# Performance work log

Measured on AMD Instinct MI355X. Metric: run time of the kernel, lower is better.

## Reference

```python
import jax, jax.numpy as jnp
import numpy as np

B, N, DIN, DOUT = 16, 256, 64, 64
TEMP = 2.0          # temperatures[0]
POOL_K = 0.5        # pool_ratios[0]
BN_EPS = 1e-5


def setup_inputs() -> dict:
    key = jax.random.key(0)
    ks = jax.random.split(key, 8)
    g = lambda i, shape: (jax.random.normal(ks[i], shape, jnp.float32) * 0.08)
    return {
        "x": jax.random.normal(ks[0], (B, N, DIN), jnp.float32),
        # GraphAttentionLayer params
        "W_att": g(1, (DIN, DOUT)), "b_att": jnp.zeros((DOUT,), jnp.float32),
        "att_w": g(2, (DOUT,)),                      # att_weight [DOUT,1] squeezed
        "W_pwa": g(3, (DIN, DOUT)), "b_pwa": jnp.zeros((DOUT,), jnp.float32),
        "W_pna": g(4, (DIN, DOUT)), "b_pna": jnp.zeros((DOUT,), jnp.float32),
        "bn_scale": jnp.ones((DOUT,), jnp.float32),
        "bn_bias": jnp.zeros((DOUT,), jnp.float32),
        # GraphPool params
        "pool_w": g(5, (DOUT,)), "pool_b": jnp.zeros((), jnp.float32),
    }


def reference(x, W_att, b_att, att_w, W_pwa, b_pwa, W_pna, b_pna,
              bn_scale, bn_bias, pool_w, pool_b):
    # --- GraphAttentionLayer (eval mode: dropout = identity) ---
    # pairwise node multiplication: [B, i, j, DIN]
    pm = x[:, :, None, :] * x[:, None, :, :]
    att = jnp.tanh(jnp.einsum('bijd,de->bije', pm, W_att) + b_att)   # [B,N,N,DOUT]
    logits = jnp.einsum('bije,e->bij', att, att_w) / TEMP            # [B,N,N]
    # torch softmax over dim=-2 of [B,i,j,1] == axis j (the aggregated axis)
    A = jax.nn.softmax(logits, axis=2)                               # [B,N,N]
    agg = jnp.einsum('bij,bjd->bid', A, x)                           # [B,N,DIN]
    h = (agg @ W_pwa + b_pwa) + (x @ W_pna + b_pna)                  # [B,N,DOUT]
    # BatchNorm1d eval with running_mean=0, running_var=1
    h = h * (bn_scale / jnp.sqrt(1.0 + BN_EPS)) + bn_bias
    h = jax.nn.selu(h)
    # --- GraphPool (eval mode: dropout = identity) ---
    scores = jax.nn.sigmoid(h @ pool_w + pool_b)                     # [B,N]
    k = max(int(N * POOL_K), 1)
    _, idx = jax.lax.top_k(scores, k)                                # [B,k]
    hw = h * scores[:, :, None]
    out = jnp.take_along_axis(hw, idx[:, :, None], axis=1)           # [B,k,DOUT]
    return out
```

## Files before the change

kernel.cpp:

```cpp
#include <hip/hip_runtime.h>
#include <hip/hip_bf16.h>
#include <math.h>

#define BB 16
#define NN 256
#define DD 64
#define KTOP 128

typedef short s16x8 __attribute__((ext_vector_type(8)));
typedef float f32x4 __attribute__((ext_vector_type(4)));

typedef union { s16x8 v; unsigned u[4]; } frag_u;
typedef union { __hip_bfloat162 b2; unsigned u; } cvu;

__device__ __forceinline__ float asf(unsigned u){ union{unsigned u;float f;}c; c.u=u; return c.f; }

__device__ __forceinline__ void split2(float v0, float v1, unsigned& hu, unsigned& lu) {
    cvu c; c.b2 = __float22bfloat162_rn(make_float2(v0, v1));
    unsigned h = c.u;
    float l0 = v0 - asf(h << 16);
    float l1 = v1 - asf(h & 0xffff0000u);
    c.b2 = __float22bfloat162_rn(make_float2(l0, l1));
    hu = h; lu = c.u;
}

__global__ __launch_bounds__(256, 2) void k_fused(
    const float* __restrict__ x, const float* __restrict__ W_att,
    const float* __restrict__ b_att, const float* __restrict__ att_w,
    const float* __restrict__ Wpwa, const float* __restrict__ bpwa,
    const float* __restrict__ Wpna, const float* __restrict__ bpna,
    const float* __restrict__ bnsc, const float* __restrict__ bnbi,
    const float* __restrict__ poolw, const float* __restrict__ poolb,
    float* __restrict__ hbuf, float* __restrict__ scores)
{
    const int ig = blockIdx.x;
    const int b  = blockIdx.y;
    const int tid = threadIdx.x;
    const int w = tid >> 6, lane = tid & 63;
    const int quad = lane >> 4, c16 = lane & 15;
    const int jb = w * 64;
    const int ibase = ig * 4;

    __shared__ float sWt[64 * 68];
    __shared__ float sXi[4 * 64];
    __shared__ float sL[4][256];
    __shared__ float sAgg[4][64];

    #pragma unroll
    for (int r = 0; r < 16; ++r) {
        int lin = r * 256 + tid;
        int d = lin >> 6, e = lin & 63;
        sWt[e * 68 + d] = W_att[lin];
    }
    sXi[tid] = x[(b * NN + ibase + (tid >> 6)) * DD + (tid & 63)];

    const float L2E2 = 2.8853900817779268f;
    float bawL[4], aww[4];
    #pragma unroll
    for (int et = 0; et < 4; ++et) {
        bawL[et] = b_att[et * 16 + c16] * L2E2;
        aww[et]  = att_w[et * 16 + c16];
    }

    frag_u Ah[4][2], Al[4][2];
    #pragma unroll
    for (int jt = 0; jt < 4; ++jt) {
        #pragma unroll
        for (int ks = 0; ks < 2; ++ks) {
            const float* xr = &x[(b * NN + jb + jt * 16 + c16) * DD + ks * 32 + quad * 8];
            float4 a0 = *(const float4*)xr;
            float4 a1 = *(const float4*)(xr + 4);
            split2(a0.x, a0.y, Ah[jt][ks].u[0], Al[jt][ks].u[0]);
            split2(a0.z, a0.w, Ah[jt][ks].u[1], Al[jt][ks].u[1]);
            split2(a1.x, a1.y, Ah[jt][ks].u[2], Al[jt][ks].u[2]);
            split2(a1.z, a1.w, Ah[jt][ks].u[3], Al[jt][ks].u[3]);
        }
    }
    __syncthreads();

    for (int ii = 0; ii < 4; ++ii) {
        float xi[2][8];
        #pragma unroll
        for (int ks = 0; ks < 2; ++ks) {
            const float* xr = &sXi[ii * 64 + ks * 32 + quad * 8];
            float4 c0 = *(const float4*)xr;
            float4 c1 = *(const float4*)(xr + 4);
            xi[ks][0]=c0.x; xi[ks][1]=c0.y; xi[ks][2]=c0.z; xi[ks][3]=c0.w;
            xi[ks][4]=c1.x; xi[ks][5]=c1.y; xi[ks][6]=c1.z; xi[ks][7]=c1.w;
        }

        f32x4 acc[4][4];
        #pragma unroll
        for (int jt = 0; jt < 4; ++jt)
            #pragma unroll
            for (int et = 0; et < 4; ++et)
                acc[jt][et] = (f32x4){0.f, 0.f, 0.f, 0.f};

        #pragma unroll
        for (int ks = 0; ks < 2; ++ks) {
            #pragma unroll
            for (int et = 0; et < 4; ++et) {
                const float* wrow = &sWt[(et * 16 + c16) * 68 + ks * 32 + quad * 8];
                float4 w0 = *(const float4*)wrow;
                float4 w1 = *(const float4*)(wrow + 4);
                frag_u bh, bl;
                split2(w0.x * xi[ks][0], w0.y * xi[ks][1], bh.u[0], bl.u[0]);
                split2(w0.z * xi[ks][2], w0.w * xi[ks][3], bh.u[1], bl.u[1]);
                split2(w1.x * xi[ks][4], w1.y * xi[ks][5], bh.u[2], bl.u[2]);
                split2(w1.z * xi[ks][6], w1.w * xi[ks][7], bh.u[3], bl.u[3]);
                #pragma unroll
                for (int jt = 0; jt < 4; ++jt) {
                    acc[jt][et] = __builtin_amdgcn_mfma_f32_16x16x32_bf16(Ah[jt][ks].v, bh.v, acc[jt][et], 0, 0, 0);
                    acc[jt][et] = __builtin_amdgcn_mfma_f32_16x16x32_bf16(Al[jt][ks].v, bh.v, acc[jt][et], 0, 0, 0);
                    acc[jt][et] = __builtin_amdgcn_mfma_f32_16x16x32_bf16(Ah[jt][ks].v, bl.v, acc[jt][et], 0, 0, 0);
                }
            }
        }

        float p[4][4];
        #pragma unroll
        for (int jt = 0; jt < 4; ++jt)
            #pragma unroll
            for (int r = 0; r < 4; ++r) p[jt][r] = 0.0f;

        #pragma unroll
        for (int et = 0; et < 4; ++et) {
            #pragma unroll
            for (int jt = 0; jt < 4; ++jt) {
                #pragma unroll
                for (int r = 0; r < 4; ++r) {
                    float arg = fmaf(acc[jt][et][r], L2E2, bawL[et]);
                    float m = __builtin_amdgcn_exp2f(arg);
                    float th = fmaf(-2.0f, __builtin_amdgcn_rcpf(m + 1.0f), 1.0f);
                    p[jt][r] = fmaf(aww[et], th, p[jt][r]);
                }
            }
        }

        #pragma unroll
        for (int jt = 0; jt < 4; ++jt) {
            #pragma unroll
            for (int r = 0; r < 4; ++r) {
                float s = p[jt][r];
                s += __shfl_xor(s, 1);
                s += __shfl_xor(s, 2);
                s += __shfl_xor(s, 4);
                s += __shfl_xor(s, 8);
                if (c16 == 0) sL[ii][jb + jt * 16 + quad * 4 + r] = s * 0.5f;
            }
        }
    }
    __syncthreads();

    {
        const int i = ibase + w;
        float* row = sL[w];
        float lg0 = row[lane], lg1 = row[lane + 64], lg2 = row[lane + 128], lg3 = row[lane + 192];
        float m = fmaxf(fmaxf(lg0, lg1), fmaxf(lg2, lg3));
        #pragma unroll
        for (int off = 32; off; off >>= 1) m = fmaxf(m, __shfl_xor(m, off));
        float e0 = __expf(lg0 - m), e1 = __expf(lg1 - m), e2 = __expf(lg2 - m), e3 = __expf(lg3 - m);
        float ssum = e0 + e1 + e2 + e3;
        #pragma unroll
        for (int off = 32; off; off >>= 1) ssum += __shfl_xor(ssum, off);
        float inv = 1.0f / ssum;
        row[lane] = e0 * inv; row[lane + 64] = e1 * inv;
        row[lane + 128] = e2 * inv; row[lane + 192] = e3 * inv;
        __asm__ volatile("s_waitcnt lgkmcnt(0)" ::: "memory");

        float agg = 0.0f;
        const float4* A4 = (const float4*)row;
        const float* xb = &x[(b * NN) * DD];
        #pragma unroll 8
        for (int jq = 0; jq < 64; ++jq) {
            float4 a = A4[jq];
            int j = jq * 4;
            agg = fmaf(a.x, xb[(j + 0) * DD + lane], agg);
            agg = fmaf(a.y, xb[(j + 1) * DD + lane], agg);
            agg = fmaf(a.z, xb[(j + 2) * DD + lane], agg);
            agg = fmaf(a.w, xb[(j + 3) * DD + lane], agg);
        }
        sAgg[w][lane] = agg;
        __asm__ volatile("s_waitcnt lgkmcnt(0)" ::: "memory");

        double hacc = (double)bpwa[lane] + (double)bpna[lane];
        #pragma unroll 4
        for (int d = 0; d < 64; ++d) {
            hacc += (double)sAgg[w][d] * (double)Wpwa[d * DD + lane]
                  + (double)sXi[w * 64 + d] * (double)Wpna[d * DD + lane];
        }
        const double bnmul = 0.99999500003749968750e0;
        double hb = hacc * ((double)bnsc[lane] * bnmul) + (double)bnbi[lane];
        float hf = (float)hb;
        const float LAM = 1.0507009873554805f, ALP = 1.6732632423543772f;
        float hs = hf > 0.0f ? LAM * hf : LAM * ALP * (__expf(hf) - 1.0f);
        hbuf[((b * NN) + i) * DD + lane] = hs;

        double z = (double)hs * (double)poolw[lane];
        #pragma unroll
        for (int off = 32; off; off >>= 1) z += __shfl_xor(z, off);
        if (lane == 0) {
            double zz = z + (double)poolb[0];
            scores[b * NN + i] = (float)(1.0 / (1.0 + exp(-zz)));
        }
    }
}

__global__ __launch_bounds__(256) void k_topk(
    const float* __restrict__ scores, const float* __restrict__ hbuf,
    float* __restrict__ out)
{
    const int b = blockIdx.x;
    const int t = threadIdx.x;
    __shared__ float ss[256];
    __shared__ int   perm[KTOP];
    ss[t] = scores[b * NN + t];
    __syncthreads();
    const float my = ss[t];
    int rank = 0;
    #pragma unroll 8
    for (int j = 0; j < 256; ++j) {
        float v = ss[j];
        rank += (v > my) || (v == my && j < t);
    }
    if (rank < KTOP) perm[rank] = t;
    __syncthreads();
    #pragma unroll
    for (int m = t; m < KTOP * DD; m += 256) {
        int r = m >> 6, e = m & 63;
        int i = perm[r];
        out[(b * KTOP + r) * DD + e] = hbuf[((b * NN) + i) * DD + e] * ss[i];
    }
}

extern "C" void kernel_launch(void* const* d_in, const int* in_sizes, int n_in,
                              void* d_out, int out_size, void* d_ws, size_t ws_size,
                              hipStream_t stream) {
    const float* x        = (const float*)d_in[0];
    const float* W_att    = (const float*)d_in[1];
    const float* b_att    = (const float*)d_in[2];
    const float* att_w    = (const float*)d_in[3];
    const float* W_pwa    = (const float*)d_in[4];
    const float* b_pwa    = (const float*)d_in[5];
    const float* W_pna    = (const float*)d_in[6];
    const float* b_pna    = (const float*)d_in[7];
    const float* bn_scale = (const float*)d_in[8];
    const float* bn_bias  = (const float*)d_in[9];
    const float* pool_w   = (const float*)d_in[10];
    const float* pool_b   = (const float*)d_in[11];

    float* hbuf    = (float*)d_ws;
    float* scoresW = hbuf + BB * NN * DD;
    float* out     = (float*)d_out;

    k_fused<<<dim3(64, BB), 256, 0, stream>>>(x, W_att, b_att, att_w,
                                              W_pwa, b_pwa, W_pna, b_pna,
                                              bn_scale, bn_bias, pool_w, pool_b,
                                              hbuf, scoresW);
    k_topk<<<dim3(BB), 256, 0, stream>>>(scoresW, hbuf, out);
}
```

Baseline: 154.8 us.

## Share split B fragments via LDS and halve accumulator live range for occupancy

Result: no change. 157.0 us (+1.4%).

```diff
diff --git a/kernel.cpp b/kernel.cpp
--- a/kernel.cpp
+++ b/kernel.cpp
@@ -24,7 +24,7 @@
     hu = h; lu = c.u;
 }
 
-__global__ __launch_bounds__(256, 2) void k_fused(
+__global__ __launch_bounds__(256, 3) void k_fused(
     const float* __restrict__ x, const float* __restrict__ W_att,
     const float* __restrict__ b_att, const float* __restrict__ att_w,
     const float* __restrict__ Wpwa, const float* __restrict__ bpwa,
@@ -41,17 +41,11 @@
     const int jb = w * 64;
     const int ibase = ig * 4;
 
-    __shared__ float sWt[64 * 68];
+    __shared__ s16x8 sB[2][4][2][64];
     __shared__ float sXi[4 * 64];
     __shared__ float sL[4][256];
     __shared__ float sAgg[4][64];
 
-    #pragma unroll
-    for (int r = 0; r < 16; ++r) {
-        int lin = r * 256 + tid;
-        int d = lin >> 6, e = lin & 63;
-        sWt[e * 68 + d] = W_att[lin];
-    }
     sXi[tid] = x[(b * NN + ibase + (tid >> 6)) * DD + (tid & 63)];
 
     const float L2E2 = 2.8853900817779268f;
@@ -79,60 +73,69 @@
     __syncthreads();
 
     for (int ii = 0; ii < 4; ++ii) {
-        float xi[2][8];
         #pragma unroll
         for (int ks = 0; ks < 2; ++ks) {
             const float* xr = &sXi[ii * 64 + ks * 32 + quad * 8];
             float4 c0 = *(const float4*)xr;
             float4 c1 = *(const float4*)(xr + 4);
-            xi[ks][0]=c0.x; xi[ks][1]=c0.y; xi[ks][2]=c0.z; xi[ks][3]=c0.w;
-            xi[ks][4]=c1.x; xi[ks][5]=c1.y; xi[ks][6]=c1.z; xi[ks][7]=c1.w;
-        }
-
-        f32x4 acc[4][4];
+            float xiv[8] = {c0.x,c0.y,c0.z,c0.w,c1.x,c1.y,c1.z,c1.w};
+            const float* wp = &W_att[(ks * 32 + quad * 8) * 64 + w * 16 + c16];
+            float wv[8];
+            #pragma unroll
+            for (int t = 0; t < 8; ++t) wv[t] = wp[t * 64];
+            frag_u bh, bl;
+            split2(wv[0] * xiv[0], wv[1] * xiv[1], bh.u[0], bl.u[0]);
+            split2(wv[2] * xiv[2], wv[3] * xiv[3], bh.u[1], bl.u[1]);
+            split2(wv[4] * xiv[4], wv[5] * xiv[5], bh.u[2], bl.u[2]);
+            split2(wv[6] * xiv[6], wv[7] * xiv[7], bh.u[3], bl.u[3]);
+            sB[ks][w][0][lane] = bh.v;
+            sB[ks][w][1][lane] = bl.v;
+        }
+        __syncthreads();
+
+        float p[4][4];
         #pragma unroll
         for (int jt = 0; jt < 4; ++jt)
             #pragma unroll
-            for (int et = 0; et < 4; ++et)
-                acc[jt][et] = (f32x4){0.f, 0.f, 0.f, 0.f};
-
-        #pragma unroll
-        for (int ks = 0; ks < 2; ++ks) {
-            #pragma unroll
-            for (int et = 0; et < 4; ++et) {
-                const float* wrow = &sWt[(et * 16 + c16) * 68 + ks * 32 + quad * 8];
-                float4 w0 = *(const float4*)wrow;
-                float4 w1 = *(const float4*)(wrow + 4);
-                frag_u bh, bl;
-                split2(w0.x * xi[ks][0], w0.y * xi[ks][1], bh.u[0], bl.u[0]);
-                split2(w0.z * xi[ks][2], w0.w * xi[ks][3], bh.u[1], bl.u[1]);
-                split2(w1.x * xi[ks][4], w1.y * xi[ks][5], bh.u[2], bl.u[2]);
-                split2(w1.z * xi[ks][6], w1.w * xi[ks][7], bh.u[3], bl.u[3]);
+            for (int r = 0; r < 4; ++r) p[jt][r] = 0.0f;
+
+        #pragma unroll
+        for (int eth = 0; eth < 2; ++eth) {
+            f32x4 acc[4][2];
+            #pragma unroll
+            for (int jt = 0; jt < 4; ++jt)
+                #pragma unroll
+                for (int e2 = 0; e2 < 2; ++e2)
+                    acc[jt][e2] = (f32x4){0.f, 0.f, 0.f, 0.f};
+
+            #pragma unroll
+            for (int ks = 0; ks < 2; ++ks) {
+                #pragma unroll
+                for (int e2 = 0; e2 < 2; ++e2) {
+                    const int et = eth * 2 + e2;
+                    s16x8 bh = sB[ks][et][0][lane];
+                    s16x8 bl = sB[ks][et][1][lane];
+                    #pragma unroll
+                    for (int jt = 0; jt < 4; ++jt) {
+                        acc[jt][e2] = __builtin_amdgcn_mfma_f32_16x16x32_bf16(Ah[jt][ks].v, bh, acc[jt][e2], 0, 0, 0);
+                        acc[jt][e2] = __builtin_amdgcn_mfma_f32_16x16x32_bf16(Al[jt][ks].v, bh, acc[jt][e2], 0, 0, 0);
+                        acc[jt][e2] = __builtin_amdgcn_mfma_f32_16x16x32_bf16(Ah[jt][ks].v, bl, acc[jt][e2], 0, 0, 0);
+                    }
+                }
+            }
+
+            #pragma unroll
+            for (int e2 = 0; e2 < 2; ++e2) {
+                const int et = eth * 2 + e2;
                 #pragma unroll
                 for (int jt = 0; jt < 4; ++jt) {
-                    acc[jt][et] = __builtin_amdgcn_mfma_f32_16x16x32_bf16(Ah[jt][ks].v, bh.v, acc[jt][et], 0, 0, 0);
-                    acc[jt][et] = __builtin_amdgcn_mfma_f32_16x16x32_bf16(Al[jt][ks].v, bh.v, acc[jt][et], 0, 0, 0);
-                    acc[jt][et] = __builtin_amdgcn_mfma_f32_16x16x32_bf16(Ah[jt][ks].v, bl.v, acc[jt][et], 0, 0, 0);
-                }
-            }
-        }
-
-        float p[4][4];
-        #pragma unroll
-        for (int jt = 0; jt < 4; ++jt)
-            #pragma unroll
-            for (int r = 0; r < 4; ++r) p[jt][r] = 0.0f;
-
-        #pragma unroll
-        for (int et = 0; et < 4; ++et) {
-            #pragma unroll
-            for (int jt = 0; jt < 4; ++jt) {
-                #pragma unroll
-                for (int r = 0; r < 4; ++r) {
-                    float arg = fmaf(acc[jt][et][r], L2E2, bawL[et]);
-                    float m = __builtin_amdgcn_exp2f(arg);
-                    float th = fmaf(-2.0f, __builtin_amdgcn_rcpf(m + 1.0f), 1.0f);
-                    p[jt][r] = fmaf(aww[et], th, p[jt][r]);
+                    #pragma unroll
+                    for (int r = 0; r < 4; ++r) {
+                        float arg = fmaf(acc[jt][e2][r], L2E2, bawL[et]);
+                        float m = __builtin_amdgcn_exp2f(arg);
+                        float th = fmaf(-2.0f, __builtin_amdgcn_rcpf(m + 1.0f), 1.0f);
+                        p[jt][r] = fmaf(aww[et], th, p[jt][r]);
+                    }
                 }
             }
         }
@@ -149,8 +152,8 @@
                 if (c16 == 0) sL[ii][jb + jt * 16 + quad * 4 + r] = s * 0.5f;
             }
         }
-    }
-    __syncthreads();
+        __syncthreads();
+    }
 
     {
         const int i = ibase + w;
```
